# Optimization experiments

Measured on AMD Instinct MI355X. Metric: run time of the kernel, lower is better.

Reference implementation:

```python
import jax, jax.numpy as jnp
import numpy as np

V_IN, V_OUT = 128, 128
E_IN, E_OUT = 64, 64
H, L, D = 256, 2, 2
DEC_H = D * L * H  # 1024
S_IN, B, S_OUT = 128, 512, 64


def _lstm_step(h, c, x, W_ih, W_hh, b):
    # PyTorch gate order: i, f, g, o
    gates = x @ W_ih.T + h @ W_hh.T + b
    i, f, g, o = jnp.split(gates, 4, axis=-1)
    c = jax.nn.sigmoid(f) * c + jax.nn.sigmoid(i) * jnp.tanh(g)
    h = jax.nn.sigmoid(o) * jnp.tanh(c)
    return h, c


def _run_lstm_dir(x_seq, W_ih, W_hh, b, reverse):
    # x_seq: [S, B, in]; returns hidden sequence [S, B, H], final (h, c)
    Bsz = x_seq.shape[1]
    Hd = W_hh.shape[1]
    init = (jnp.zeros((Bsz, Hd), x_seq.dtype), jnp.zeros((Bsz, Hd), x_seq.dtype))

    def step(carry, x):
        h, c = _lstm_step(carry[0], carry[1], x, W_ih, W_hh, b)
        return (h, c), h

    (hf, cf), hs = jax.lax.scan(step, init, x_seq, reverse=reverse)
    return hs, hf, cf


def setup_inputs() -> dict:
    key = jax.random.key(0)
    ks = jax.random.split(key, 20)
    s = 0.05
    inp = {}
    inp["input_tokens"] = jax.random.randint(ks[0], (S_IN, B), 0, V_IN, dtype=jnp.int32)
    inp["output_tokens"] = jax.random.randint(ks[1], (B, S_OUT), 0, V_OUT, dtype=jnp.int32)
    inp["in_emb"] = jax.random.normal(ks[2], (V_IN, E_IN), jnp.float32) * s
    # encoder layer 0: input E_IN; layer 1: input D*H. Leading dim 2 = directions.
    inp["enc_W_ih0"] = jax.random.normal(ks[3], (2, 4 * H, E_IN), jnp.float32) * s
    inp["enc_W_hh0"] = jax.random.normal(ks[4], (2, 4 * H, H), jnp.float32) * s
    inp["enc_b0"] = jax.random.normal(ks[5], (2, 4 * H), jnp.float32) * s
    inp["enc_W_ih1"] = jax.random.normal(ks[6], (2, 4 * H, D * H), jnp.float32) * s
    inp["enc_W_hh1"] = jax.random.normal(ks[7], (2, 4 * H, H), jnp.float32) * s
    inp["enc_b1"] = jax.random.normal(ks[8], (2, 4 * H), jnp.float32) * s
    inp["out_emb"] = jax.random.normal(ks[9], (V_OUT, E_OUT), jnp.float32) * s
    inp["dec_W_ih"] = jax.random.normal(ks[10], (4 * DEC_H, E_OUT), jnp.float32) * s
    inp["dec_W_hh"] = jax.random.normal(ks[11], (4 * DEC_H, DEC_H), jnp.float32) * s
    inp["dec_b"] = jax.random.normal(ks[12], (4 * DEC_H,), jnp.float32) * s
    inp["proj_W"] = jax.random.normal(ks[13], (V_OUT, DEC_H), jnp.float32) * s
    inp["proj_b"] = jax.random.normal(ks[14], (V_OUT,), jnp.float32) * s
    return inp


def reference(input_tokens, output_tokens, in_emb,
              enc_W_ih0, enc_W_hh0, enc_b0,
              enc_W_ih1, enc_W_hh1, enc_b1,
              out_emb, dec_W_ih, dec_W_hh, dec_b, proj_W, proj_b):
    # ---- encoder: 2-layer bidirectional LSTM over [S_in, B] ----
    x = in_emb[input_tokens]  # [S, B, E_IN]
    h_list, c_list = [], []
    for W_ih, W_hh, b in ((enc_W_ih0, enc_W_hh0, enc_b0),
                          (enc_W_ih1, enc_W_hh1, enc_b1)):
        hs_f, hf, cf = _run_lstm_dir(x, W_ih[0], W_hh[0], b[0], False)
        hs_b, hb, cb = _run_lstm_dir(x, W_ih[1], W_hh[1], b[1], True)
        x = jnp.concatenate([hs_f, hs_b], axis=-1)  # [S, B, 2H]
        h_list += [hf, hb]
        c_list += [cf, cb]
    Bsz = x.shape[1]
    # PyTorch h_n order: (l0_fwd, l0_bwd, l1_fwd, l1_bwd) -> swapaxes+reshape
    h0 = jnp.stack(h_list, axis=1).reshape(Bsz, -1)  # [B, D*L*H]
    c0 = jnp.stack(c_list, axis=1).reshape(Bsz, -1)

    # ---- decoder: teacher-forced LSTMCell loop ----
    tok_in = output_tokens[:, :-1].T   # [T-1, B]
    tok_next = output_tokens[:, 1:].T  # [T-1, B]

    def step(carry, toks):
        h, c = carry
        t_in, t_next = toks
        e = out_emb[t_in]                                 # [B, E_OUT]
        h, c = _lstm_step(h, c, e, dec_W_ih, dec_W_hh, dec_b)
        logits = c @ proj_W.T + proj_b                    # NOTE: proj on CELL, as in source
        greedy = jnp.argmax(logits, axis=1)
        lp = jax.nn.log_softmax(logits, axis=-1)
        logp = jnp.take_along_axis(lp, t_next[:, None], axis=1)[:, 0]
        return (h, c), (greedy, logp)

    _, (decoded_tokens, log_probs) = jax.lax.scan(step, (h0, c0), (tok_in, tok_next))
    cum_log_probs = jnp.sum(log_probs, axis=0)  # [B]
    return decoded_tokens, cum_log_probs
```

## Files before the change

### kernel.cpp

```cpp
#include <hip/hip_runtime.h>
#include <math.h>

#define B 512
#define S_IN 128
#define S_OUT 64
#define T_DEC 63

#define O_H0   0
#define O_C    (512*1024)
#define O_H1   (2*512*1024)
#define O_CUM  (3*512*1024)
#define O_HS0  (O_CUM + 512)
#define O_PWT  (O_HS0 + 128*512*512)
#define WS_FLOATS (O_PWT + 1024*128)

template<int MODE>
__global__ __launch_bounds__(256)
void step_kernel(const float* __restrict__ Wih, const float* __restrict__ Whh,
                 const float* __restrict__ bias,
                 const int* __restrict__ tok, const float* __restrict__ emb,
                 const float* __restrict__ seqin,
                 const float* __restrict__ h_in, float* __restrict__ h_out,
                 float* __restrict__ c_st, float* __restrict__ seqout, int t)
{
    constexpr int KE = (MODE==0) ? 64 : (MODE==1 ? 512 : 64);
    constexpr int KH = (MODE==2) ? 1024 : 256;
    constexpr int K  = KE + KH;
    constexpr int N  = (MODE==2) ? 4096 : 1024;
    constexpr int HH = N/4;
    constexpr int NK = K/16;

    const int dir   = (MODE==2) ? 0 : blockIdx.z;
    const int t_eff = (MODE==2) ? t : (dir ? (S_IN-1-t) : t);
    const int hseg  = (MODE==0) ? dir*256 : (MODE==1 ? 512 + dir*256 : 0);

    const float* Wih_d = Wih + (size_t)dir*N*KE;
    const float* Whh_d = Whh + (size_t)dir*N*KH;
    const float* b_d   = bias + dir*N;

    __shared__ float As[16][64];
    __shared__ float Bs[16][64];

    const int tid = threadIdx.x;
    const int bm0 = blockIdx.x*64;
    const int bn0 = blockIdx.y*64;

    const int la_m  = tid >> 2;
    const int la_k  = (tid & 3) << 2;
    const int a_row = bm0 + la_m;

    const int lb_n = tid >> 2;
    const int lb_k = (tid & 3) << 2;
    const int n_g  = bn0 + lb_n;
    const int b_j  = (n_g & 3)*HH + (n_g >> 2);

    int tokidx = 0;
    if (MODE==0) tokidx = tok[t_eff*B + a_row];
    if (MODE==2) tokidx = tok[a_row*S_OUT + t];

    const int tm = (tid >> 4) << 2;
    const int tn = (tid & 15) << 2;

    float acc[4][4] = {};

    auto loadA = [&](int kt) -> float4 {
        int k = kt*16 + la_k;
        if (k < KE) {
            if (MODE==1) return *(const float4*)&seqin[((size_t)t_eff*B + a_row)*512 + k];
            else         return *(const float4*)&emb[(size_t)tokidx*64 + k];
        }
        return *(const float4*)&h_in[(size_t)a_row*1024 + hseg + (k-KE)];
    };
    auto loadB = [&](int kt) -> float4 {
        int k = kt*16 + lb_k;
        if (k < KE) return *(const float4*)&Wih_d[(size_t)b_j*KE + k];
        return *(const float4*)&Whh_d[(size_t)b_j*KH + (k-KE)];
    };

    float4 aR = loadA(0), bR = loadB(0);
    for (int kt=0; kt<NK; ++kt) {
        __syncthreads();
        As[la_k+0][la_m]=aR.x; As[la_k+1][la_m]=aR.y; As[la_k+2][la_m]=aR.z; As[la_k+3][la_m]=aR.w;
        Bs[lb_k+0][lb_n]=bR.x; Bs[lb_k+1][lb_n]=bR.y; Bs[lb_k+2][lb_n]=bR.z; Bs[lb_k+3][lb_n]=bR.w;
        __syncthreads();
        if (kt+1 < NK) { aR = loadA(kt+1); bR = loadB(kt+1); }
        #pragma unroll
        for (int k=0;k<16;k++){
            const float4 a = *(const float4*)&As[k][tm];
            const float4 b = *(const float4*)&Bs[k][tn];
            acc[0][0]+=a.x*b.x; acc[0][1]+=a.x*b.y; acc[0][2]+=a.x*b.z; acc[0][3]+=a.x*b.w;
            acc[1][0]+=a.y*b.x; acc[1][1]+=a.y*b.y; acc[1][2]+=a.y*b.z; acc[1][3]+=a.y*b.w;
            acc[2][0]+=a.z*b.x; acc[2][1]+=a.z*b.y; acc[2][2]+=a.z*b.z; acc[2][3]+=a.z*b.w;
            acc[3][0]+=a.w*b.x; acc[3][1]+=a.w*b.y; acc[3][2]+=a.w*b.z; acc[3][3]+=a.w*b.w;
        }
    }

    const int jh = (bn0 + tn) >> 2;
    const float bi = b_d[0*HH + jh];
    const float bf = b_d[1*HH + jh];
    const float bg = b_d[2*HH + jh];
    const float bo = b_d[3*HH + jh];
    #pragma unroll
    for (int i=0;i<4;i++){
        const int brow = bm0 + tm + i;
        float xi = acc[i][0] + bi;
        float xf = acc[i][1] + bf;
        float xg = acc[i][2] + bg;
        float xo = acc[i][3] + bo;
        float ig = 1.f/(1.f+expf(-xi));
        float fg = 1.f/(1.f+expf(-xf));
        float gg = tanhf(xg);
        float og = 1.f/(1.f+expf(-xo));
        size_t ci = (size_t)brow*1024 + hseg + jh;
        float cn = fg*c_st[ci] + ig*gg;
        float hn = og*tanhf(cn);
        c_st[ci]  = cn;
        h_out[ci] = hn;
        if (MODE==0) seqout[((size_t)t_eff*B + brow)*512 + dir*256 + jh] = hn;
    }
}

__global__ __launch_bounds__(128)
void proj_kernel(const float* __restrict__ c, const float* __restrict__ wT,
                 const float* __restrict__ pb, const int* __restrict__ out_tok,
                 float* __restrict__ cum, float* __restrict__ dout, int t)
{
    __shared__ float cs[4][1024];
    __shared__ float ls[4][128];
    const int tid = threadIdx.x;
    const int b0 = blockIdx.x*4;
    #pragma unroll
    for (int r=0;r<4;r++){
        #pragma unroll
        for (int q=0;q<2;q++){
            int k = (q*128 + tid)*4;
            *(float4*)&cs[r][k] = *(const float4*)&c[((size_t)(b0+r))*1024 + k];
        }
    }
    __syncthreads();
    float a0=0.f,a1=0.f,a2=0.f,a3=0.f;
    for (int k=0;k<1024;k++){
        float w = wT[k*128 + tid];
        a0 += w*cs[0][k]; a1 += w*cs[1][k]; a2 += w*cs[2][k]; a3 += w*cs[3][k];
    }
    float bb = pb[tid];
    ls[0][tid]=a0+bb; ls[1][tid]=a1+bb; ls[2][tid]=a2+bb; ls[3][tid]=a3+bb;
    __syncthreads();
    if (tid < 4){
        const int r = tid, b = b0 + r;
        float m = ls[r][0]; int am = 0;
        for (int j=1;j<128;j++){ float v=ls[r][j]; if (v>m){m=v;am=j;} }
        float s=0.f;
        for (int j=0;j<128;j++) s += expf(ls[r][j]-m);
        int tnx = out_tok[b*S_OUT + t + 1];
        float logp = ls[r][tnx] - m - logf(s);
        float cn = ((t==0)?0.f:cum[b]) + logp;
        cum[b] = cn;
        dout[T_DEC*B + b] = cn;
        dout[t*B + b] = (float)am;
    }
}

__global__ void transpose_proj(const float* __restrict__ W, float* __restrict__ WT){
    int idx = blockIdx.x*blockDim.x + threadIdx.x;
    if (idx < 1024*128){
        int j = idx & 127, k = idx >> 7;
        WT[idx] = W[j*1024 + k];
    }
}

__global__ void zero_kernel(float* __restrict__ p, int n){
    int i = blockIdx.x*blockDim.x + threadIdx.x;
    if (i < n) p[i] = 0.f;
}

extern "C" void kernel_launch(void* const* d_in, const int* in_sizes, int n_in,
                              void* d_out, int out_size, void* d_ws, size_t ws_size,
                              hipStream_t stream)
{
    const int*   input_tokens  = (const int*)d_in[0];
    const int*   output_tokens = (const int*)d_in[1];
    const float* in_emb  = (const float*)d_in[2];
    const float* eWih0   = (const float*)d_in[3];
    const float* eWhh0   = (const float*)d_in[4];
    const float* eb0     = (const float*)d_in[5];
    const float* eWih1   = (const float*)d_in[6];
    const float* eWhh1   = (const float*)d_in[7];
    const float* eb1     = (const float*)d_in[8];
    const float* out_emb = (const float*)d_in[9];
    const float* dWih    = (const float*)d_in[10];
    const float* dWhh    = (const float*)d_in[11];
    const float* db      = (const float*)d_in[12];
    const float* pW      = (const float*)d_in[13];
    const float* pb      = (const float*)d_in[14];

    if (ws_size < (size_t)WS_FLOATS * 4) return;

    float* ws  = (float*)d_ws;
    float* out = (float*)d_out;

    float* h[2] = { ws + O_H0, ws + O_H1 };
    float* c    = ws + O_C;
    float* cum  = ws + O_CUM;
    float* hs0  = ws + O_HS0;
    float* pwt  = ws + O_PWT;

    zero_kernel<<<4096,256,0,stream>>>(ws, 2*512*1024);
    transpose_proj<<<512,256,0,stream>>>(pW, pwt);

    for (int t=0;t<S_IN;t++)
        step_kernel<0><<<dim3(8,16,2),256,0,stream>>>(eWih0, eWhh0, eb0,
            input_tokens, in_emb, nullptr, h[t&1], h[(t+1)&1], c, hs0, t);

    for (int t=0;t<S_IN;t++)
        step_kernel<1><<<dim3(8,16,2),256,0,stream>>>(eWih1, eWhh1, eb1,
            nullptr, nullptr, hs0, h[t&1], h[(t+1)&1], c, nullptr, t);

    for (int t=0;t<T_DEC;t++){
        step_kernel<2><<<dim3(8,64,1),256,0,stream>>>(dWih, dWhh, db,
            output_tokens, out_emb, nullptr, h[t&1], h[(t+1)&1], c, nullptr, t);
        proj_kernel<<<128,128,0,stream>>>(c, pwt, pb, output_tokens, cum, out, t);
    }
}
```

Baseline: 21.08 ms.

## Precompute encoder layer-1 input gates in chunks, retile decoder GEMM, rework projection

```diff
diff --git a/kernel.cpp b/kernel.cpp
--- a/kernel.cpp
+++ b/kernel.cpp
@@ -7,36 +7,32 @@
 #define T_DEC 63
 
 #define O_H0   0
-#define O_C    (512*1024)
-#define O_H1   (2*512*1024)
+#define O_H1   (512*1024)
+#define O_C    (2*512*1024)
 #define O_CUM  (3*512*1024)
 #define O_HS0  (O_CUM + 512)
-#define O_PWT  (O_HS0 + 128*512*512)
-#define WS_FLOATS (O_PWT + 1024*128)
+#define O_P1   (O_HS0 + 128*512*512)
 
 template<int MODE>
 __global__ __launch_bounds__(256)
-void step_kernel(const float* __restrict__ Wih, const float* __restrict__ Whh,
-                 const float* __restrict__ bias,
-                 const int* __restrict__ tok, const float* __restrict__ emb,
-                 const float* __restrict__ seqin,
-                 const float* __restrict__ h_in, float* __restrict__ h_out,
-                 float* __restrict__ c_st, float* __restrict__ seqout, int t)
+void enc_step(const float* __restrict__ Wih, const float* __restrict__ Whh,
+              const float* __restrict__ bias, const int* __restrict__ tok,
+              const float* __restrict__ emb, const float* __restrict__ seqin,
+              const float* __restrict__ h_in, float* __restrict__ h_out,
+              float* __restrict__ c_st, float* __restrict__ seqout,
+              const float* __restrict__ p1, int t)
 {
-    constexpr int KE = (MODE==0) ? 64 : (MODE==1 ? 512 : 64);
-    constexpr int KH = (MODE==2) ? 1024 : 256;
-    constexpr int K  = KE + KH;
-    constexpr int N  = (MODE==2) ? 4096 : 1024;
-    constexpr int HH = N/4;
+    constexpr int KE = (MODE==0) ? 64 : (MODE==2 ? 512 : 0);
+    constexpr int K  = KE + 256;
     constexpr int NK = K/16;
 
-    const int dir   = (MODE==2) ? 0 : blockIdx.z;
-    const int t_eff = (MODE==2) ? t : (dir ? (S_IN-1-t) : t);
-    const int hseg  = (MODE==0) ? dir*256 : (MODE==1 ? 512 + dir*256 : 0);
-
-    const float* Wih_d = Wih + (size_t)dir*N*KE;
-    const float* Whh_d = Whh + (size_t)dir*N*KH;
-    const float* b_d   = bias + dir*N;
+    const int dir   = blockIdx.z;
+    const int t_eff = dir ? (S_IN-1-t) : t;
+    const int hseg  = (MODE==0) ? dir*256 : 512 + dir*256;
+
+    const float* Wih_d = Wih + (size_t)dir*1024*KE;
+    const float* Whh_d = Whh + (size_t)dir*1024*256;
+    const float* b_d   = bias + dir*1024;
 
     __shared__ float As[16][64];
     __shared__ float Bs[16][64];
@@ -52,11 +48,10 @@
     const int lb_n = tid >> 2;
     const int lb_k = (tid & 3) << 2;
     const int n_g  = bn0 + lb_n;
-    const int b_j  = (n_g & 3)*HH + (n_g >> 2);
+    const int b_j  = (n_g & 3)*256 + (n_g >> 2);
 
     int tokidx = 0;
     if (MODE==0) tokidx = tok[t_eff*B + a_row];
-    if (MODE==2) tokidx = tok[a_row*S_OUT + t];
 
     const int tm = (tid >> 4) << 2;
     const int tn = (tid & 15) << 2;
@@ -65,16 +60,20 @@
 
     auto loadA = [&](int kt) -> float4 {
         int k = kt*16 + la_k;
-        if (k < KE) {
-            if (MODE==1) return *(const float4*)&seqin[((size_t)t_eff*B + a_row)*512 + k];
-            else         return *(const float4*)&emb[(size_t)tokidx*64 + k];
-        }
-        return *(const float4*)&h_in[(size_t)a_row*1024 + hseg + (k-KE)];
+        if (MODE==0) {
+            if (k < 64) return *(const float4*)&emb[(size_t)tokidx*64 + k];
+            return *(const float4*)&h_in[(size_t)a_row*1024 + hseg + (k-64)];
+        } else if (MODE==2) {
+            if (k < 512) return *(const float4*)&seqin[((size_t)t_eff*B + a_row)*512 + k];
+            return *(const float4*)&h_in[(size_t)a_row*1024 + hseg + (k-512)];
+        } else {
+            return *(const float4*)&h_in[(size_t)a_row*1024 + hseg + k];
+        }
     };
     auto loadB = [&](int kt) -> float4 {
         int k = kt*16 + lb_k;
-        if (k < KE) return *(const float4*)&Wih_d[(size_t)b_j*KE + k];
-        return *(const float4*)&Whh_d[(size_t)b_j*KH + (k-KE)];
+        if (KE && k < KE) return *(const float4*)&Wih_d[(size_t)b_j*KE + k];
+        return *(const float4*)&Whh_d[(size_t)b_j*256 + (k-KE)];
     };
 
     float4 aR = loadA(0), bR = loadB(0);
@@ -96,10 +95,10 @@
     }
 
     const int jh = (bn0 + tn) >> 2;
-    const float bi = b_d[0*HH + jh];
-    const float bf = b_d[1*HH + jh];
-    const float bg = b_d[2*HH + jh];
-    const float bo = b_d[3*HH + jh];
+    const float bi = b_d[0*256 + jh];
+    const float bf = b_d[1*256 + jh];
+    const float bg = b_d[2*256 + jh];
+    const float bo = b_d[3*256 + jh];
     #pragma unroll
     for (int i=0;i<4;i++){
         const int brow = bm0 + tm + i;
@@ -107,6 +106,10 @@
         float xf = acc[i][1] + bf;
         float xg = acc[i][2] + bg;
         float xo = acc[i][3] + bo;
+        if (MODE==1) {
+            const float4 pv = *(const float4*)&p1[((size_t)dir*512 + brow)*1024 + bn0 + tn];
+            xi += pv.x; xf += pv.y; xg += pv.z; xo += pv.w;
+        }
         float ig = 1.f/(1.f+expf(-xi));
         float fg = 1.f/(1.f+expf(-xf));
         float gg = tanhf(xg);
@@ -120,58 +123,197 @@
     }
 }
 
+template<int MODE>
 __global__ __launch_bounds__(128)
-void proj_kernel(const float* __restrict__ c, const float* __restrict__ wT,
-                 const float* __restrict__ pb, const int* __restrict__ out_tok,
-                 float* __restrict__ cum, float* __restrict__ dout, int t)
+void gemm128(const float* __restrict__ Wih, const float* __restrict__ Whh,
+             const float* __restrict__ bias, const int* __restrict__ tok,
+             const float* __restrict__ emb, const float* __restrict__ hs0,
+             const float* __restrict__ h_in, float* __restrict__ h_out,
+             float* __restrict__ c_st, float* __restrict__ p1out, int t_or_s0)
 {
-    __shared__ float cs[4][1024];
-    __shared__ float ls[4][128];
+    constexpr int KE = (MODE==0) ? 64 : 0;
+    constexpr int K  = (MODE==0) ? 1088 : 512;
+    constexpr int NK = K/16;
+    constexpr int HH = (MODE==0) ? 1024 : 256;
+
+    const int dir = (MODE==1) ? blockIdx.z : 0;
+
+    __shared__ float As[16][64];
+    __shared__ float Bs[16][64];
+
     const int tid = threadIdx.x;
-    const int b0 = blockIdx.x*4;
+    const int bm0 = blockIdx.x*64;
+    const int bn0 = blockIdx.y*64;
+
+    const int la_m  = tid >> 1;
+    const int la_k  = (tid & 1) << 3;
+    const int a_row = bm0 + la_m;
+
+    const int srel  = (MODE==1) ? (blockIdx.x >> 3) : 0;
+    const int sabs  = (MODE==1) ? (t_or_s0 + srel) : 0;
+    const int t_eff = (MODE==1) ? (dir ? (S_IN-1-sabs) : sabs) : 0;
+    const int a_b   = a_row & 511;
+
+    const int n_g = bn0 + la_m;
+    const int b_j = (n_g & 3)*HH + (n_g >> 2);
+
+    const float* Wih_d = (MODE==1) ? (Wih + (size_t)dir*1024*512) : Wih;
+
+    int tokidx = 0;
+    if (MODE==0) tokidx = tok[a_row*S_OUT + t_or_s0];
+
+    const int tm = (tid >> 3) << 2;
+    const int tn = (tid & 7) << 3;
+
+    float acc[4][8] = {};
+
+    auto loadA = [&](int kt, int q) -> float4 {
+        int k = kt*16 + la_k + q*4;
+        if (MODE==0) {
+            if (k < 64) return *(const float4*)&emb[(size_t)tokidx*64 + k];
+            return *(const float4*)&h_in[(size_t)a_row*1024 + (k-64)];
+        }
+        return *(const float4*)&hs0[((size_t)t_eff*B + a_b)*512 + k];
+    };
+    auto loadB = [&](int kt, int q) -> float4 {
+        int k = kt*16 + la_k + q*4;
+        if (MODE==0) {
+            if (k < 64) return *(const float4*)&Wih[(size_t)b_j*64 + k];
+            return *(const float4*)&Whh[(size_t)b_j*1024 + (k-64)];
+        }
+        return *(const float4*)&Wih_d[(size_t)b_j*512 + k];
+    };
+
+    float4 aR0 = loadA(0,0), aR1 = loadA(0,1);
+    float4 bR0 = loadB(0,0), bR1 = loadB(0,1);
+    for (int kt=0; kt<NK; ++kt) {
+        __syncthreads();
+        As[la_k+0][la_m]=aR0.x; As[la_k+1][la_m]=aR0.y; As[la_k+2][la_m]=aR0.z; As[la_k+3][la_m]=aR0.w;
+        As[la_k+4][la_m]=aR1.x; As[la_k+5][la_m]=aR1.y; As[la_k+6][la_m]=aR1.z; As[la_k+7][la_m]=aR1.w;
+        Bs[la_k+0][la_m]=bR0.x; Bs[la_k+1][la_m]=bR0.y; Bs[la_k+2][la_m]=bR0.z; Bs[la_k+3][la_m]=bR0.w;
+        Bs[la_k+4][la_m]=bR1.x; Bs[la_k+5][la_m]=bR1.y; Bs[la_k+6][la_m]=bR1.z; Bs[la_k+7][la_m]=bR1.w;
+        __syncthreads();
+        if (kt+1 < NK) {
+            aR0 = loadA(kt+1,0); aR1 = loadA(kt+1,1);
+            bR0 = loadB(kt+1,0); bR1 = loadB(kt+1,1);
+        }
+        #pragma unroll
+        for (int k=0;k<16;k++){
+            const float4 a  = *(const float4*)&As[k][tm];
+            const float4 b0 = *(const float4*)&Bs[k][tn];
+            const float4 b1 = *(const float4*)&Bs[k][tn+4];
+            acc[0][0]+=a.x*b0.x; acc[0][1]+=a.x*b0.y; acc[0][2]+=a.x*b0.z; acc[0][3]+=a.x*b0.w;
+            acc[0][4]+=a.x*b1.x; acc[0][5]+=a.x*b1.y; acc[0][6]+=a.x*b1.z; acc[0][7]+=a.x*b1.w;
+            acc[1][0]+=a.y*b0.x; acc[1][1]+=a.y*b0.y; acc[1][2]+=a.y*b0.z; acc[1][3]+=a.y*b0.w;
+            acc[1][4]+=a.y*b1.x; acc[1][5]+=a.y*b1.y; acc[1][6]+=a.y*b1.z; acc[1][7]+=a.y*b1.w;
+            acc[2][0]+=a.z*b0.x; acc[2][1]+=a.z*b0.y; acc[2][2]+=a.z*b0.z; acc[2][3]+=a.z*b0.w;
+            acc[2][4]+=a.z*b1.x; acc[2][5]+=a.z*b1.y; acc[2][6]+=a.z*b1.z; acc[2][7]+=a.z*b1.w;
+            acc[3][0]+=a.w*b0.x; acc[3][1]+=a.w*b0.y; acc[3][2]+=a.w*b0.z; acc[3][3]+=a.w*b0.w;
+            acc[3][4]+=a.w*b1.x; acc[3][5]+=a.w*b1.y; acc[3][6]+=a.w*b1.z; acc[3][7]+=a.w*b1.w;
+        }
+    }
+
+    if (MODE==0) {
+        const int jh0 = (bn0 + tn) >> 2;
+        #pragma unroll
+        for (int u=0;u<2;u++){
+            const int jh = jh0 + u;
+            const float bi = bias[0*1024 + jh];
+            const float bf = bias[1*1024 + jh];
+            const float bg = bias[2*1024 + jh];
+            const float bo = bias[3*1024 + jh];
+            #pragma unroll
+            for (int i=0;i<4;i++){
+                const int brow = bm0 + tm + i;
+                float xi = acc[i][4*u+0] + bi;
+                float xf = acc[i][4*u+1] + bf;
+                float xg = acc[i][4*u+2] + bg;
+                float xo = acc[i][4*u+3] + bo;
+                float ig = 1.f/(1.f+expf(-xi));
+                float fg = 1.f/(1.f+expf(-xf));
+                float gg = tanhf(xg);
+                float og = 1.f/(1.f+expf(-xo));
+                size_t ci = (size_t)brow*1024 + jh;
+                float cn = fg*c_st[ci] + ig*gg;
+                float hn = og*tanhf(cn);
+                c_st[ci]  = cn;
+                h_out[ci] = hn;
+            }
+        }
+    } else {
+        #pragma unroll
+        for (int i=0;i<4;i++){
+            const int r = bm0 + tm + i;
+            size_t base = ((size_t)(srel*2 + dir)*512 + (r & 511))*1024 + bn0 + tn;
+            *(float4*)&p1out[base]   = *(float4*)&acc[i][0];
+            *(float4*)&p1out[base+4] = *(float4*)&acc[i][4];
+        }
+    }
+}
+
+__global__ __launch_bounds__(256)
+void proj2(const float* __restrict__ c, const float* __restrict__ pW,
+           const float* __restrict__ pb, const int* __restrict__ out_tok,
+           float* __restrict__ cum, float* __restrict__ dout, int t)
+{
+    __shared__ float cs[8][1024];
+    __shared__ float ls[8][128];
+    const int tid = threadIdx.x;
+    const int b0 = blockIdx.x*8;
     #pragma unroll
-    for (int r=0;r<4;r++){
-        #pragma unroll
-        for (int q=0;q<2;q++){
-            int k = (q*128 + tid)*4;
-            *(float4*)&cs[r][k] = *(const float4*)&c[((size_t)(b0+r))*1024 + k];
-        }
-    }
+    for (int r=0;r<8;r++)
+        *(float4*)&cs[r][tid*4] = *(const float4*)&c[(size_t)(b0+r)*1024 + tid*4];
     __syncthreads();
+
+    const int wave = tid >> 6, lane = tid & 63;
+    const int col  = wave*32 + (lane & 31);
+    const int rb   = (lane >> 5) * 4;
     float a0=0.f,a1=0.f,a2=0.f,a3=0.f;
-    for (int k=0;k<1024;k++){
-        float w = wT[k*128 + tid];
-        a0 += w*cs[0][k]; a1 += w*cs[1][k]; a2 += w*cs[2][k]; a3 += w*cs[3][k];
-    }
-    float bb = pb[tid];
-    ls[0][tid]=a0+bb; ls[1][tid]=a1+bb; ls[2][tid]=a2+bb; ls[3][tid]=a3+bb;
+    for (int k=0;k<1024;k+=4){
+        const float4 w = *(const float4*)&pW[(size_t)col*1024 + k];
+        const float4 c0 = *(const float4*)&cs[rb+0][k];
+        const float4 c1 = *(const float4*)&cs[rb+1][k];
+        const float4 c2 = *(const float4*)&cs[rb+2][k];
+        const float4 c3 = *(const float4*)&cs[rb+3][k];
+        a0 += w.x*c0.x + w.y*c0.y + w.z*c0.z + w.w*c0.w;
+        a1 += w.x*c1.x + w.y*c1.y + w.z*c1.z + w.w*c1.w;
+        a2 += w.x*c2.x + w.y*c2.y + w.z*c2.z + w.w*c2.w;
+        a3 += w.x*c3.x + w.y*c3.y + w.z*c3.z + w.w*c3.w;
+    }
+    const float bb = pb[col];
+    ls[rb+0][col]=a0+bb; ls[rb+1][col]=a1+bb; ls[rb+2][col]=a2+bb; ls[rb+3][col]=a3+bb;
     __syncthreads();
-    if (tid < 4){
-        const int r = tid, b = b0 + r;
-        float m = ls[r][0]; int am = 0;
-        for (int j=1;j<128;j++){ float v=ls[r][j]; if (v>m){m=v;am=j;} }
-        float s=0.f;
-        for (int j=0;j<128;j++) s += expf(ls[r][j]-m);
-        int tnx = out_tok[b*S_OUT + t + 1];
-        float logp = ls[r][tnx] - m - logf(s);
-        float cn = ((t==0)?0.f:cum[b]) + logp;
-        cum[b] = cn;
-        dout[T_DEC*B + b] = cn;
-        dout[t*B + b] = (float)am;
-    }
-}
-
-__global__ void transpose_proj(const float* __restrict__ W, float* __restrict__ WT){
-    int idx = blockIdx.x*blockDim.x + threadIdx.x;
-    if (idx < 1024*128){
-        int j = idx & 127, k = idx >> 7;
-        WT[idx] = W[j*1024 + k];
-    }
-}
-
-__global__ void zero_kernel(float* __restrict__ p, int n){
+
+    #pragma unroll
+    for (int rr=0;rr<2;rr++){
+        const int r = wave*2 + rr, b = b0 + r;
+        float v0 = ls[r][lane], v1 = ls[r][lane+64];
+        float mv; int mi;
+        if (v1 > v0) { mv = v1; mi = lane+64; } else { mv = v0; mi = lane; }
+        #pragma unroll
+        for (int o=32;o>=1;o>>=1){
+            float ov = __shfl_xor(mv, o);
+            int   oi = __shfl_xor(mi, o);
+            if (ov > mv || (ov == mv && oi < mi)) { mv = ov; mi = oi; }
+        }
+        float e = expf(v0 - mv) + expf(v1 - mv);
+        #pragma unroll
+        for (int o=32;o>=1;o>>=1) e += __shfl_xor(e, o);
+        if (lane == 0){
+            const int tnx = out_tok[b*S_OUT + t + 1];
+            const float lv = ls[r][tnx];
+            const float logp = lv - mv - logf(e);
+            const float cn = ((t==0) ? 0.f : cum[b]) + logp;
+            cum[b] = cn;
+            dout[T_DEC*B + b] = cn;
+            dout[t*B + b] = (float)mi;
+        }
+    }
+}
+
+__global__ void zero_kernel(float* __restrict__ p, int n4){
     int i = blockIdx.x*blockDim.x + threadIdx.x;
-    if (i < n) p[i] = 0.f;
+    if (i < n4) *(float4*)&p[i*4] = float4{0.f,0.f,0.f,0.f};
 }
 
 extern "C" void kernel_launch(void* const* d_in, const int* in_sizes, int n_in,
@@ -194,7 +336,14 @@
     const float* pW      = (const float*)d_in[13];
     const float* pb      = (const float*)d_in[14];
 
-    if (ws_size < (size_t)WS_FLOATS * 4) return;
+    size_t ws_fl = ws_size / 4;
+    if (ws_fl < (size_t)O_P1) return;
+
+    int CH = 0;
+    if      (ws_fl >= (size_t)O_P1 + 16u*1048576u) CH = 16;
+    else if (ws_fl >= (size_t)O_P1 +  8u*1048576u) CH = 8;
+    else if (ws_fl >= (size_t)O_P1 +  4u*1048576u) CH = 4;
+    else if (ws_fl >= (size_t)O_P1 +  2u*1048576u) CH = 2;
 
     float* ws  = (float*)d_ws;
     float* out = (float*)d_out;
@@ -203,22 +352,32 @@
     float* c    = ws + O_C;
     float* cum  = ws + O_CUM;
     float* hs0  = ws + O_HS0;
-    float* pwt  = ws + O_PWT;
-
-    zero_kernel<<<4096,256,0,stream>>>(ws, 2*512*1024);
-    transpose_proj<<<512,256,0,stream>>>(pW, pwt);
+    float* p1   = ws + O_P1;
+
+    zero_kernel<<<(O_HS0/4 + 255)/256, 256, 0, stream>>>(ws, O_HS0/4);
 
     for (int t=0;t<S_IN;t++)
-        step_kernel<0><<<dim3(8,16,2),256,0,stream>>>(eWih0, eWhh0, eb0,
-            input_tokens, in_emb, nullptr, h[t&1], h[(t+1)&1], c, hs0, t);
-
-    for (int t=0;t<S_IN;t++)
-        step_kernel<1><<<dim3(8,16,2),256,0,stream>>>(eWih1, eWhh1, eb1,
-            nullptr, nullptr, hs0, h[t&1], h[(t+1)&1], c, nullptr, t);
+        enc_step<0><<<dim3(8,16,2),256,0,stream>>>(eWih0, eWhh0, eb0,
+            input_tokens, in_emb, nullptr, h[t&1], h[(t+1)&1], c, hs0, nullptr, t);
+
+    if (CH) {
+        for (int s0=0; s0<S_IN; s0+=CH) {
+            gemm128<1><<<dim3(CH*8,16,2),128,0,stream>>>(eWih1, nullptr, nullptr,
+                nullptr, nullptr, hs0, nullptr, nullptr, nullptr, p1, s0);
+            for (int s=s0; s<s0+CH; ++s)
+                enc_step<1><<<dim3(8,16,2),256,0,stream>>>(eWih1, eWhh1, eb1,
+                    nullptr, nullptr, nullptr, h[s&1], h[(s+1)&1], c, nullptr,
+                    p1 + (size_t)(s-s0)*2*512*1024, s);
+        }
+    } else {
+        for (int t=0;t<S_IN;t++)
+            enc_step<2><<<dim3(8,16,2),256,0,stream>>>(eWih1, eWhh1, eb1,
+                nullptr, nullptr, hs0, h[t&1], h[(t+1)&1], c, nullptr, nullptr, t);
+    }
 
     for (int t=0;t<T_DEC;t++){
-        step_kernel<2><<<dim3(8,64,1),256,0,stream>>>(dWih, dWhh, db,
+        gemm128<0><<<dim3(8,64,1),128,0,stream>>>(dWih, dWhh, db,
             output_tokens, out_emb, nullptr, h[t&1], h[(t+1)&1], c, nullptr, t);
-        proj_kernel<<<128,128,0,stream>>>(c, pwt, pb, output_tokens, cum, out, t);
-    }
-}
+        proj2<<<64,256,0,stream>>>(c, pW, pb, output_tokens, cum, out, t);
+    }
+}
```

Result: faster. 16.89 ms (-19.9%).
